# Kernel tuning notes

Hardware: AMD Instinct MI355X
Metric: run time of the kernel (lower is better)

The kernel has to match this reference:

```python
import jax, jax.numpy as jnp
import numpy as np

N_NODES = 100000
N_EDGES = 600000
D = 128


def setup_inputs() -> dict:
    key = jax.random.key(0)
    k1, k2, k3, k4, k5, k6 = jax.random.split(key, 6)
    feat = jax.random.normal(k1, (N_NODES, D), dtype=jnp.float32)
    src = jax.random.randint(k2, (N_EDGES,), 0, N_NODES, dtype=jnp.int64)
    dst = jax.random.randint(k3, (N_EDGES,), 0, N_NODES, dtype=jnp.int64)
    W_neigh = jax.random.normal(k4, (D, D), dtype=jnp.float32) * (1.0 / np.sqrt(D))
    b_neigh = jax.random.normal(k5, (D,), dtype=jnp.float32) * 0.02
    W_self = jax.random.normal(k6, (D, D), dtype=jnp.float32) * (1.0 / np.sqrt(D))
    return {"feat": feat, "src": src, "dst": dst,
            "W_neigh": W_neigh, "b_neigh": b_neigh, "W_self": W_self}


def reference(feat, src, dst, W_neigh, b_neigh, W_self):
    # DGL GraphConv(norm='none'): sum-aggregate neighbor features, then linear.
    # agg[i] = sum_{(s->i) in E} feat[s]
    agg = jax.ops.segment_sum(feat[src], dst, num_segments=feat.shape[0])  # [N, D]
    neigh_feat = agg @ W_neigh + b_neigh                                   # [N, Dout]
    self_feat = feat @ W_self                                              # [N, Dout]
    return neigh_feat + self_feat
```

## Files before the change

### kernel.cpp

```cpp
#include <hip/hip_runtime.h>

#define DF 128
#define CAP 16
#define GR 64

typedef __attribute__((ext_vector_type(8))) short short8;
typedef __attribute__((ext_vector_type(4))) float v4f;

__device__ __forceinline__ unsigned short f2bf(float x) {
    unsigned u = __float_as_uint(x);
    unsigned r = (u + 0x7FFFu + ((u >> 16) & 1u)) >> 16;
    return (unsigned short)r;
}
__device__ __forceinline__ float bf2f(unsigned short h) {
    return __uint_as_float((unsigned)h << 16);
}
__device__ __forceinline__ unsigned pack2(float a, float b) {
    return (unsigned)f2bf(a) | ((unsigned)f2bf(b) << 16);
}

__global__ __launch_bounds__(128) void detect_idx_kernel(
    const int* __restrict__ idx32, int n, int* __restrict__ flag32)
{
    int t = threadIdx.x;
    int found = 0;
    for (int i = t; i < 2048 && i < n; i += 128) {
        if (idx32[2 * i + 1] != 0) found = 1;
    }
    if (__any(found) && (t & 63) == 0) atomicOr(flag32, 1);
}

__global__ __launch_bounds__(256) void prep_w_kernel(
    const float* __restrict__ Wn, const float* __restrict__ Ws,
    unsigned short* __restrict__ Bt)
{
    int idx = blockIdx.x * 256 + threadIdx.x;
    int n = idx >> 7, k = idx & 127;
    float v = (n < DF) ? Wn[(size_t)k * DF + n] : Ws[(size_t)k * DF + (n - DF)];
    Bt[idx] = f2bf(v);
}

__global__ __launch_bounds__(256) void gemm_kernel(
    const float* __restrict__ feat, const unsigned short* __restrict__ Bt,
    const float* __restrict__ bias, unsigned short* __restrict__ Ybf,
    float* __restrict__ out, int M)
{
    __shared__ unsigned short As[GR][136];
    __shared__ unsigned short Ys[GR][136];

    const int t = threadIdx.x;
    const int wave = t >> 6;
    const int lane = t & 63;
    const int nl   = lane & 15;
    const int quad = lane >> 4;
    const int block_row = blockIdx.x * GR;

    {
        const float* base = feat + (size_t)block_row * DF;
#pragma unroll
        for (int it = 0; it < 8; it++) {
            const int idx = t * 4 + it * 1024;
            const int row = idx >> 7, col = idx & 127;
            float4 v;
            if (block_row + row < M)
                v = *reinterpret_cast<const float4*>(base + idx);
            else
                v = make_float4(0.f, 0.f, 0.f, 0.f);
            uint2 pk;
            pk.x = pack2(v.x, v.y);
            pk.y = pack2(v.z, v.w);
            *reinterpret_cast<uint2*>(&As[row][col]) = pk;
        }
    }

    const int n0 = wave * 64;
    short8 bfrag[4][4];
#pragma unroll
    for (int ct = 0; ct < 4; ct++)
#pragma unroll
        for (int kk = 0; kk < 4; kk++)
            bfrag[ct][kk] = *reinterpret_cast<const short8*>(
                Bt + (size_t)(n0 + ct * 16 + nl) * DF + kk * 32 + quad * 8);

    float bcol[4];
#pragma unroll
    for (int ct = 0; ct < 4; ct++) {
        int n = n0 + ct * 16 + nl;
        bcol[ct] = (n >= DF) ? bias[n - DF] : 0.f;
    }

    __syncthreads();

#pragma unroll
    for (int rt = 0; rt < 4; rt++) {
        short8 afrag[4];
#pragma unroll
        for (int kk = 0; kk < 4; kk++)
            afrag[kk] = *reinterpret_cast<const short8*>(
                &As[rt * 16 + nl][kk * 32 + quad * 8]);
#pragma unroll
        for (int ct = 0; ct < 4; ct++) {
            v4f acc = {0.f, 0.f, 0.f, 0.f};
#pragma unroll
            for (int kk = 0; kk < 4; kk++)
                acc = __builtin_amdgcn_mfma_f32_16x16x32_bf16(
                    afrag[kk], bfrag[ct][kk], acc, 0, 0, 0);
            const int n = n0 + ct * 16 + nl;
            const int lrow = rt * 16 + quad * 4;
            if (n < DF) {
#pragma unroll
                for (int r = 0; r < 4; r++)
                    Ys[lrow + r][n] = f2bf(acc[r]);
            } else {
#pragma unroll
                for (int r = 0; r < 4; r++) {
                    const int grow = block_row + lrow + r;
                    if (grow < M)
                        out[(size_t)grow * DF + (n - DF)] = acc[r] + bcol[ct];
                }
            }
        }
    }

    __syncthreads();

    {
        const int row = t >> 2;
        const int cb  = (t & 3) * 32;
        const int grow = block_row + row;
        if (grow < M) {
            const uint4* srcp = reinterpret_cast<const uint4*>(&Ys[row][cb]);
            uint4* dstp = reinterpret_cast<uint4*>(Ybf + (size_t)grow * DF + cb);
            dstp[0] = srcp[0];
            dstp[1] = srcp[1];
            dstp[2] = srcp[2];
            dstp[3] = srcp[3];
        }
    }
}

__global__ __launch_bounds__(256) void placement_kernel(
    const void* __restrict__ src, const void* __restrict__ dst,
    int* __restrict__ counts, int* __restrict__ buckets,
    const unsigned short* __restrict__ Ybf, float* __restrict__ out,
    int nE, const int* __restrict__ flag32)
{
    int e = blockIdx.x * 256 + threadIdx.x;
    if (e >= nE) return;
    long long s, d;
    if (*flag32) {
        s = ((const int*)src)[e];
        d = ((const int*)dst)[e];
    } else {
        s = ((const long long*)src)[e];
        d = ((const long long*)dst)[e];
    }

    int pos = atomicAdd(&counts[d], 1);
    if (pos < CAP) {
        buckets[(size_t)d * CAP + pos] = (int)s;
    } else {
        const unsigned short* yr = Ybf + (size_t)s * DF;
        float* orow = out + (size_t)d * DF;
        for (int i = 0; i < DF; i++)
            unsafeAtomicAdd(orow + i, bf2f(yr[i]));
    }
}

__global__ __launch_bounds__(256) void gather_kernel(
    const unsigned short* __restrict__ Ybf,
    const int* __restrict__ counts, const int* __restrict__ buckets,
    float* __restrict__ out, int M)
{
    int gid = blockIdx.x * 256 + threadIdx.x;
    int node = gid >> 5;
    if (node >= M) return;
    int lane = gid & 31;

    int deg = counts[node];
    if (deg > CAP) deg = CAP;
    const int* b = buckets + (size_t)node * CAP;

    float4 acc = make_float4(0.f, 0.f, 0.f, 0.f);
    int e = 0;
    for (; e + 4 <= deg; e += 4) {
        int4 ss = *reinterpret_cast<const int4*>(b + e);
        ushort4 y0 = *reinterpret_cast<const ushort4*>(Ybf + (size_t)ss.x * DF + lane * 4);
        ushort4 y1 = *reinterpret_cast<const ushort4*>(Ybf + (size_t)ss.y * DF + lane * 4);
        ushort4 y2 = *reinterpret_cast<const ushort4*>(Ybf + (size_t)ss.z * DF + lane * 4);
        ushort4 y3 = *reinterpret_cast<const ushort4*>(Ybf + (size_t)ss.w * DF + lane * 4);
        acc.x += (bf2f(y0.x) + bf2f(y1.x)) + (bf2f(y2.x) + bf2f(y3.x));
        acc.y += (bf2f(y0.y) + bf2f(y1.y)) + (bf2f(y2.y) + bf2f(y3.y));
        acc.z += (bf2f(y0.z) + bf2f(y1.z)) + (bf2f(y2.z) + bf2f(y3.z));
        acc.w += (bf2f(y0.w) + bf2f(y1.w)) + (bf2f(y2.w) + bf2f(y3.w));
    }
    for (; e < deg; e++) {
        int s0 = b[e];
        ushort4 y0 = *reinterpret_cast<const ushort4*>(Ybf + (size_t)s0 * DF + lane * 4);
        acc.x += bf2f(y0.x);
        acc.y += bf2f(y0.y);
        acc.z += bf2f(y0.z);
        acc.w += bf2f(y0.w);
    }

    float* op = out + (size_t)node * DF + lane * 4;
    float4 o = *reinterpret_cast<const float4*>(op);
    o.x += acc.x; o.y += acc.y; o.z += acc.z; o.w += acc.w;
    *reinterpret_cast<float4*>(op) = o;
}

extern "C" void kernel_launch(void* const* d_in, const int* in_sizes, int n_in,
                              void* d_out, int out_size, void* d_ws, size_t ws_size,
                              hipStream_t stream) {
    const float* feat = (const float*)d_in[0];
    const void*  src  = d_in[1];
    const void*  dst  = d_in[2];
    const float* Wn   = (const float*)d_in[3];
    const float* bias = (const float*)d_in[4];
    const float* Wsf  = (const float*)d_in[5];
    float* out = (float*)d_out;

    const int M  = in_sizes[0] / DF;
    const int nE = in_sizes[1];

    const size_t cnt_off   = 256;
    const size_t cnt_bytes = (((size_t)(M + 1) * 4) + 255) & ~(size_t)255;
    const size_t bkt_off   = cnt_off + cnt_bytes;
    const size_t bkt_bytes = (size_t)M * CAP * sizeof(int);
    const size_t bt_off    = (bkt_off + bkt_bytes + 255) & ~(size_t)255;
    const size_t bt_bytes  = (size_t)256 * DF * sizeof(unsigned short);
    const size_t y_off     = bt_off + bt_bytes;

    int*            flag    = (int*)d_ws;
    int*            counts  = (int*)((char*)d_ws + cnt_off);
    int*            buckets = (int*)((char*)d_ws + bkt_off);
    unsigned short* Bt      = (unsigned short*)((char*)d_ws + bt_off);
    unsigned short* Ybf     = (unsigned short*)((char*)d_ws + y_off);

    hipMemsetAsync(d_ws, 0, cnt_off + cnt_bytes, stream);

    detect_idx_kernel<<<1, 128, 0, stream>>>((const int*)src, nE, flag);

    prep_w_kernel<<<128, 256, 0, stream>>>(Wn, Wsf, Bt);

    const int gemm_blocks = (M + GR - 1) / GR;
    gemm_kernel<<<gemm_blocks, 256, 0, stream>>>(feat, Bt, bias, Ybf, out, M);

    const int pblocks = (nE + 255) / 256;
    placement_kernel<<<pblocks, 256, 0, stream>>>(
        src, dst, counts, buckets, Ybf, out, nE, flag);

    const int gablocks = (int)(((long long)M * 32 + 255) / 256);
    gather_kernel<<<gablocks, 256, 0, stream>>>(Ybf, counts, buckets, out, M);
}
```

Baseline: 221.0 us.

## Fuse prep kernels and edge placement into GEMM, defer overflow edges to gather

Merges index-width detection, weight transpose and counts zeroing into a single prep kernel, which replaces the memset and two small launches. Edge bucketing moves into the tail of the GEMM kernel, so each block places a slice of edges after its GEMM work and the separate placement launch goes away. Edges beyond the bucket cap are appended to an overflow list and accumulated with atomics inside the gather kernel. Nodes that overflowed add their bucketed sum with atomics to avoid racing with those overflow adds. The intent is to cut launch count and the serialized per-row atomic loop in placement, at the cost of a longer GEMM kernel and extra atomics on the overflow list.

```diff
diff --git a/kernel.cpp b/kernel.cpp
--- a/kernel.cpp
+++ b/kernel.cpp
@@ -19,31 +19,42 @@
     return (unsigned)f2bf(a) | ((unsigned)f2bf(b) << 16);
 }
 
-__global__ __launch_bounds__(128) void detect_idx_kernel(
-    const int* __restrict__ idx32, int n, int* __restrict__ flag32)
+__global__ __launch_bounds__(256) void prep_kernel(
+    const int* __restrict__ idx32, int nE, int* __restrict__ hdr,
+    const float* __restrict__ Wn, const float* __restrict__ Ws,
+    unsigned short* __restrict__ Bt, int* __restrict__ counts, int cnt_ints)
 {
-    int t = threadIdx.x;
-    int found = 0;
-    for (int i = t; i < 2048 && i < n; i += 128) {
-        if (idx32[2 * i + 1] != 0) found = 1;
-    }
-    if (__any(found) && (t & 63) == 0) atomicOr(flag32, 1);
-}
-
-__global__ __launch_bounds__(256) void prep_w_kernel(
-    const float* __restrict__ Wn, const float* __restrict__ Ws,
-    unsigned short* __restrict__ Bt)
-{
-    int idx = blockIdx.x * 256 + threadIdx.x;
-    int n = idx >> 7, k = idx & 127;
-    float v = (n < DF) ? Wn[(size_t)k * DF + n] : Ws[(size_t)k * DF + (n - DF)];
-    Bt[idx] = f2bf(v);
-}
-
-__global__ __launch_bounds__(256) void gemm_kernel(
+    const int b = blockIdx.x;
+    const int t = threadIdx.x;
+    if (b == 0) {
+        __shared__ int sh;
+        if (t == 0) sh = 0;
+        __syncthreads();
+        int found = 0;
+        for (int i = t; i < 2048 && i < nE; i += 256)
+            if (idx32[2 * i + 1] != 0) found = 1;
+        if (found) sh = 1;
+        __syncthreads();
+        if (t == 0) { hdr[0] = sh; hdr[1] = 0; }
+    } else if (b <= 128) {
+        int idx = (b - 1) * 256 + t;
+        int n = idx >> 7, k = idx & 127;
+        float v = (n < DF) ? Wn[(size_t)k * DF + n] : Ws[(size_t)k * DF + (n - DF)];
+        Bt[idx] = f2bf(v);
+    } else {
+        int off = ((b - 129) * 256 + t) * 4;
+        if (off < cnt_ints)
+            *reinterpret_cast<int4*>(counts + off) = make_int4(0, 0, 0, 0);
+    }
+}
+
+__global__ __launch_bounds__(256) void gemmplace_kernel(
     const float* __restrict__ feat, const unsigned short* __restrict__ Bt,
     const float* __restrict__ bias, unsigned short* __restrict__ Ybf,
-    float* __restrict__ out, int M)
+    float* __restrict__ out, int M,
+    const void* __restrict__ src, const void* __restrict__ dst, int nE, int EPB,
+    int* __restrict__ hdr, int* __restrict__ counts, int* __restrict__ buckets,
+    int2* __restrict__ ovf)
 {
     __shared__ unsigned short As[GR][136];
     __shared__ unsigned short Ys[GR][136];
@@ -137,76 +148,91 @@
             dstp[3] = srcp[3];
         }
     }
-}
-
-__global__ __launch_bounds__(256) void placement_kernel(
-    const void* __restrict__ src, const void* __restrict__ dst,
-    int* __restrict__ counts, int* __restrict__ buckets,
-    const unsigned short* __restrict__ Ybf, float* __restrict__ out,
-    int nE, const int* __restrict__ flag32)
-{
-    int e = blockIdx.x * 256 + threadIdx.x;
-    if (e >= nE) return;
-    long long s, d;
-    if (*flag32) {
-        s = ((const int*)src)[e];
-        d = ((const int*)dst)[e];
-    } else {
-        s = ((const long long*)src)[e];
-        d = ((const long long*)dst)[e];
-    }
-
-    int pos = atomicAdd(&counts[d], 1);
-    if (pos < CAP) {
-        buckets[(size_t)d * CAP + pos] = (int)s;
-    } else {
-        const unsigned short* yr = Ybf + (size_t)s * DF;
-        float* orow = out + (size_t)d * DF;
-        for (int i = 0; i < DF; i++)
-            unsafeAtomicAdd(orow + i, bf2f(yr[i]));
+
+    {
+        const int is32 = hdr[0];
+        const int e_end = min(nE, (int)(blockIdx.x + 1) * EPB);
+        for (int e = blockIdx.x * EPB + t; e < e_end; e += 256) {
+            long long s, d;
+            if (is32) {
+                s = ((const int*)src)[e];
+                d = ((const int*)dst)[e];
+            } else {
+                s = ((const long long*)src)[e];
+                d = ((const long long*)dst)[e];
+            }
+            int pos = atomicAdd(&counts[d], 1);
+            if (pos < CAP) {
+                buckets[(size_t)d * CAP + pos] = (int)s;
+            } else {
+                int oi = atomicAdd(&hdr[1], 1);
+                ovf[oi] = make_int2((int)s, (int)d);
+            }
+        }
     }
 }
 
 __global__ __launch_bounds__(256) void gather_kernel(
     const unsigned short* __restrict__ Ybf,
     const int* __restrict__ counts, const int* __restrict__ buckets,
-    float* __restrict__ out, int M)
+    const int* __restrict__ hdr, const int2* __restrict__ ovf,
+    float* __restrict__ out, int M, int ngroups)
 {
     int gid = blockIdx.x * 256 + threadIdx.x;
     int node = gid >> 5;
-    if (node >= M) return;
     int lane = gid & 31;
 
-    int deg = counts[node];
-    if (deg > CAP) deg = CAP;
-    const int* b = buckets + (size_t)node * CAP;
-
-    float4 acc = make_float4(0.f, 0.f, 0.f, 0.f);
-    int e = 0;
-    for (; e + 4 <= deg; e += 4) {
-        int4 ss = *reinterpret_cast<const int4*>(b + e);
-        ushort4 y0 = *reinterpret_cast<const ushort4*>(Ybf + (size_t)ss.x * DF + lane * 4);
-        ushort4 y1 = *reinterpret_cast<const ushort4*>(Ybf + (size_t)ss.y * DF + lane * 4);
-        ushort4 y2 = *reinterpret_cast<const ushort4*>(Ybf + (size_t)ss.z * DF + lane * 4);
-        ushort4 y3 = *reinterpret_cast<const ushort4*>(Ybf + (size_t)ss.w * DF + lane * 4);
-        acc.x += (bf2f(y0.x) + bf2f(y1.x)) + (bf2f(y2.x) + bf2f(y3.x));
-        acc.y += (bf2f(y0.y) + bf2f(y1.y)) + (bf2f(y2.y) + bf2f(y3.y));
-        acc.z += (bf2f(y0.z) + bf2f(y1.z)) + (bf2f(y2.z) + bf2f(y3.z));
-        acc.w += (bf2f(y0.w) + bf2f(y1.w)) + (bf2f(y2.w) + bf2f(y3.w));
-    }
-    for (; e < deg; e++) {
-        int s0 = b[e];
-        ushort4 y0 = *reinterpret_cast<const ushort4*>(Ybf + (size_t)s0 * DF + lane * 4);
-        acc.x += bf2f(y0.x);
-        acc.y += bf2f(y0.y);
-        acc.z += bf2f(y0.z);
-        acc.w += bf2f(y0.w);
-    }
-
-    float* op = out + (size_t)node * DF + lane * 4;
-    float4 o = *reinterpret_cast<const float4*>(op);
-    o.x += acc.x; o.y += acc.y; o.z += acc.z; o.w += acc.w;
-    *reinterpret_cast<float4*>(op) = o;
+    if (node < M) {
+        int deg_raw = counts[node];
+        int deg = min(deg_raw, CAP);
+        const int* b = buckets + (size_t)node * CAP;
+
+        float4 acc = make_float4(0.f, 0.f, 0.f, 0.f);
+        int e = 0;
+        for (; e + 4 <= deg; e += 4) {
+            int4 ss = *reinterpret_cast<const int4*>(b + e);
+            ushort4 y0 = *reinterpret_cast<const ushort4*>(Ybf + (size_t)ss.x * DF + lane * 4);
+            ushort4 y1 = *reinterpret_cast<const ushort4*>(Ybf + (size_t)ss.y * DF + lane * 4);
+            ushort4 y2 = *reinterpret_cast<const ushort4*>(Ybf + (size_t)ss.z * DF + lane * 4);
+            ushort4 y3 = *reinterpret_cast<const ushort4*>(Ybf + (size_t)ss.w * DF + lane * 4);
+            acc.x += (bf2f(y0.x) + bf2f(y1.x)) + (bf2f(y2.x) + bf2f(y3.x));
+            acc.y += (bf2f(y0.y) + bf2f(y1.y)) + (bf2f(y2.y) + bf2f(y3.y));
+            acc.z += (bf2f(y0.z) + bf2f(y1.z)) + (bf2f(y2.z) + bf2f(y3.z));
+            acc.w += (bf2f(y0.w) + bf2f(y1.w)) + (bf2f(y2.w) + bf2f(y3.w));
+        }
+        for (; e < deg; e++) {
+            int s0 = b[e];
+            ushort4 y0 = *reinterpret_cast<const ushort4*>(Ybf + (size_t)s0 * DF + lane * 4);
+            acc.x += bf2f(y0.x);
+            acc.y += bf2f(y0.y);
+            acc.z += bf2f(y0.z);
+            acc.w += bf2f(y0.w);
+        }
+
+        float* op = out + (size_t)node * DF + lane * 4;
+        if (deg_raw <= CAP) {
+            float4 o = *reinterpret_cast<const float4*>(op);
+            o.x += acc.x; o.y += acc.y; o.z += acc.z; o.w += acc.w;
+            *reinterpret_cast<float4*>(op) = o;
+        } else {
+            unsafeAtomicAdd(op + 0, acc.x);
+            unsafeAtomicAdd(op + 1, acc.y);
+            unsafeAtomicAdd(op + 2, acc.z);
+            unsafeAtomicAdd(op + 3, acc.w);
+        }
+    }
+
+    int n_ovf = hdr[1];
+    for (int i = gid >> 5; i < n_ovf; i += ngroups) {
+        int2 sd = ovf[i];
+        ushort4 y = *reinterpret_cast<const ushort4*>(
+            Ybf + (size_t)sd.x * DF + lane * 4);
+        float* op = out + (size_t)sd.y * DF + lane * 4;
+        unsafeAtomicAdd(op + 0, bf2f(y.x));
+        unsafeAtomicAdd(op + 1, bf2f(y.y));
+        unsafeAtomicAdd(op + 2, bf2f(y.z));
+        unsafeAtomicAdd(op + 3, bf2f(y.w));
+    }
 }
 
 extern "C" void kernel_launch(void* const* d_in, const int* in_sizes, int n_in,
@@ -230,26 +256,29 @@
     const size_t bt_off    = (bkt_off + bkt_bytes + 255) & ~(size_t)255;
     const size_t bt_bytes  = (size_t)256 * DF * sizeof(unsigned short);
     const size_t y_off     = bt_off + bt_bytes;
-
-    int*            flag    = (int*)d_ws;
+    const size_t y_bytes   = (size_t)M * DF * sizeof(unsigned short);
+    const size_t ovf_off   = (y_off + y_bytes + 255) & ~(size_t)255;
+
+    int*            hdr     = (int*)d_ws;
     int*            counts  = (int*)((char*)d_ws + cnt_off);
     int*            buckets = (int*)((char*)d_ws + bkt_off);
     unsigned short* Bt      = (unsigned short*)((char*)d_ws + bt_off);
     unsigned short* Ybf     = (unsigned short*)((char*)d_ws + y_off);
-
-    hipMemsetAsync(d_ws, 0, cnt_off + cnt_bytes, stream);
-
-    detect_idx_kernel<<<1, 128, 0, stream>>>((const int*)src, nE, flag);
-
-    prep_w_kernel<<<128, 256, 0, stream>>>(Wn, Wsf, Bt);
+    int2*           ovf     = (int2*)((char*)d_ws + ovf_off);
+
+    const int cnt_ints = (int)(cnt_bytes / 4);
+    const int nzb = (cnt_ints + 1023) / 1024;
+    prep_kernel<<<1 + 128 + nzb, 256, 0, stream>>>(
+        (const int*)src, nE, hdr, Wn, Wsf, Bt, counts, cnt_ints);
 
     const int gemm_blocks = (M + GR - 1) / GR;
-    gemm_kernel<<<gemm_blocks, 256, 0, stream>>>(feat, Bt, bias, Ybf, out, M);
-
-    const int pblocks = (nE + 255) / 256;
-    placement_kernel<<<pblocks, 256, 0, stream>>>(
-        src, dst, counts, buckets, Ybf, out, nE, flag);
+    const int EPB = (nE + gemm_blocks - 1) / gemm_blocks;
+    gemmplace_kernel<<<gemm_blocks, 256, 0, stream>>>(
+        feat, Bt, bias, Ybf, out, M, src, dst, nE, EPB,
+        hdr, counts, buckets, ovf);
 
     const int gablocks = (int)(((long long)M * 32 + 255) / 256);
-    gather_kernel<<<gablocks, 256, 0, stream>>>(Ybf, counts, buckets, out, M);
-}
+    const int ngroups = gablocks * 8;
+    gather_kernel<<<gablocks, 256, 0, stream>>>(
+        Ybf, counts, buckets, hdr, ovf, out, M, ngroups);
+}
```

Result: faster. 209.4 us (-5.2%).
